# Performance work log

Measured on AMD Instinct MI355X. Metric: run time of the kernel, lower is better.

## Reference

```python
import jax, jax.numpy as jnp
import numpy as np

B, H, L, D = 2, 16, 2048, 64


def setup_inputs() -> dict:
    key = jax.random.key(0)
    kq, kk, kv, km = jax.random.split(key, 4)
    q = jax.random.normal(kq, (B, H, L, D), dtype=jnp.float32)
    k = jax.random.normal(kk, (B, H, L, D), dtype=jnp.float32)
    v = jax.random.normal(kv, (B, H, L, D), dtype=jnp.float32)
    mask = jax.random.uniform(km, (B, L, L), dtype=jnp.float32)
    return {"q": q, "k": k, "v": v, "mask": mask}


def reference(q, k, v, mask):
    d_tensor = k.shape[-1]
    # score = q @ k^T / sqrt(d)  -> [B,H,L,L]
    score = jnp.einsum("bhqd,bhkd->bhqk", q, k) / jnp.sqrt(jnp.float32(d_tensor))
    # multiplicative mask, broadcast over heads (mask: [B,L,L] -> [B,1,L,L])
    score = score * mask[:, None, :, :]
    score = jax.nn.softmax(score, axis=-1)
    out = jnp.einsum("bhqk,bhkd->bhqd", score, v)
    return (out, score)
```

## Files before the change

### kernel.cpp

```cpp
#include <hip/hip_runtime.h>

typedef __attribute__((ext_vector_type(8))) short bf16x8;
typedef __attribute__((ext_vector_type(4))) float f32x4;
typedef __attribute__((ext_vector_type(4))) unsigned u32x4;

#define DEV static __device__ __forceinline__

constexpr int B_ = 2, H_ = 16, L_ = 2048, D_ = 64;
constexpr float SCALE = 0.125f;

DEV short f2bf(float f) {
  unsigned u = __builtin_bit_cast(unsigned, f);
  u += 0x7fffu + ((u >> 16) & 1u);
  return (short)(u >> 16);
}
DEV unsigned pk2(float lo, float hi) {
  return (unsigned)(unsigned short)f2bf(lo) | ((unsigned)(unsigned short)f2bf(hi) << 16);
}
DEV float bflo(unsigned u) { return __builtin_bit_cast(float, u << 16); }
DEV float bfhi(unsigned u) { return __builtin_bit_cast(float, u & 0xffff0000u); }

DEV bf16x8 frag_from(const float* src) {
  float4 f0 = *(const float4*)src;
  float4 f1 = *(const float4*)(src + 4);
  bf16x8 r;
  r[0] = f2bf(f0.x); r[1] = f2bf(f0.y); r[2] = f2bf(f0.z); r[3] = f2bf(f0.w);
  r[4] = f2bf(f1.x); r[5] = f2bf(f1.y); r[6] = f2bf(f1.z); r[7] = f2bf(f1.w);
  return r;
}

__global__ __launch_bounds__(256) void convert_k_kernel(
    const float* __restrict__ Kg, short* __restrict__ Kp) {
  const int tid = threadIdx.x;
  const int lane = tid & 63, half = (tid >> 6) & 1, sub = tid >> 7;
  const int blk = blockIdx.x;
  const int bh = blk >> 6;
  const int ktile = (((blk & 63) << 1) | sub);
  const int g = lane >> 4, ln = lane & 15;
  const float* src = Kg + ((size_t)bh * L_ + ktile * 16 + ln) * D_ + half * 32 + g * 8;
  bf16x8 f = frag_from(src);
  *(bf16x8*)(Kp + ((((size_t)(bh * 128 + ktile)) * 2 + half) * 64 + lane) * 8) = f;
}

__global__ __launch_bounds__(256) void convert_vp_kernel(
    const float* __restrict__ Vg, short* __restrict__ Vp) {
  __shared__ short vt[64 * 256];
  const int tid = threadIdx.x;
  const int bh = blockIdx.x >> 3, c = blockIdx.x & 7;
  const float* vb = Vg + (size_t)bh * L_ * D_ + (size_t)c * 256 * D_;
  const int ka = (tid & 127) * 2, dh = (tid >> 7) * 32;
  const float* r0 = vb + (size_t)ka * D_ + dh;
  const float* r1 = r0 + D_;
#pragma unroll
  for (int i = 0; i < 8; ++i) {
    float4 a = *(const float4*)(r0 + i * 4);
    float4 b = *(const float4*)(r1 + i * 4);
    unsigned p0 = pk2(a.x, b.x), p1 = pk2(a.y, b.y), p2 = pk2(a.z, b.z), p3 = pk2(a.w, b.w);
    const int dd = dh + i * 4;
    *(unsigned*)((char*)vt + (dd + 0) * 512 + ((ka * 2) ^ (((dd + 0) & 7) << 4))) = p0;
    *(unsigned*)((char*)vt + (dd + 1) * 512 + ((ka * 2) ^ (((dd + 1) & 7) << 4))) = p1;
    *(unsigned*)((char*)vt + (dd + 2) * 512 + ((ka * 2) ^ (((dd + 2) & 7) << 4))) = p2;
    *(unsigned*)((char*)vt + (dd + 3) * 512 + ((ka * 2) ^ (((dd + 3) & 7) << 4))) = p3;
  }
  __syncthreads();
  u32x4* out = (u32x4*)Vp + (size_t)(bh * 8 + c) * 2048;
#pragma unroll
  for (int i = 0; i < 8; ++i) {
    const int u = tid + 256 * i;
    const int lane = u & 63, w = (u >> 6) & 7, n = u >> 9;
    const int g = lane >> 4, ln = lane & 15;
    const int d = n * 16 + ln;
    const int kb = (w * 16 + g * 4) * 2;
    const char* rowp = (const char*)vt + d * 512;
    const int swz = (d & 7) << 4;
    uint2 lo = *(const uint2*)(rowp + (kb ^ swz));
    uint2 hi = *(const uint2*)(rowp + ((kb + 256) ^ swz));
    out[u] = u32x4{lo.x, lo.y, hi.x, hi.y};
  }
}

template <bool USEPRE>
__global__ __launch_bounds__(512, 2) void attn_fused(
    const float* __restrict__ Qg, const float* __restrict__ Kg,
    const short* __restrict__ Kp, const float* __restrict__ Vg,
    const short* __restrict__ Vpg, const float* __restrict__ Mg,
    float* __restrict__ Pg, float* __restrict__ Og) {
  const int tid = threadIdx.x;
  const int w = tid >> 6, lane = tid & 63;
  const int g = lane >> 4, ln = lane & 15;

  const int bid = blockIdx.x;
  const int wg = (bid & 7) * 512 + (bid >> 3);
  const int q0 = (wg & 127) << 4;
  const int bh = wg >> 7;
  const int b = bh >> 4;

  __shared__ float red_o[128 * 64];
  __shared__ float red[8][16];

  const float* qp = Qg + (size_t)bh * L_ * D_;
  const float* mrow = Mg + (size_t)b * L_ * L_ + (size_t)(q0 + ln) * L_;
  float* prow = Pg + (size_t)bh * L_ * L_ + (size_t)(q0 + ln) * L_;

  bf16x8 qf0 = frag_from(qp + (size_t)(q0 + ln) * D_ + g * 8);
  bf16x8 qf1 = frag_from(qp + (size_t)(q0 + ln) * D_ + 32 + g * 8);

  unsigned pkv[32];
  float mx = -1e30f;
  const bf16x8* kpb = (const bf16x8*)Kp + ((size_t)bh * 128 + w) * 128 + lane;

#pragma unroll
  for (int j = 0; j < 16; ++j) {
    bf16x8 k0, k1;
    if (USEPRE) {
      k0 = kpb[j * 1024];
      k1 = kpb[j * 1024 + 64];
    } else {
      const float* kr = Kg + (size_t)bh * L_ * D_ + (size_t)((w + 8 * j) * 16 + ln) * D_;
      k0 = frag_from(kr + g * 8);
      k1 = frag_from(kr + 32 + g * 8);
    }
    f32x4 acc{0.f, 0.f, 0.f, 0.f};
    acc = __builtin_amdgcn_mfma_f32_16x16x32_bf16(k0, qf0, acc, 0, 0, 0);
    acc = __builtin_amdgcn_mfma_f32_16x16x32_bf16(k1, qf1, acc, 0, 0, 0);
    float4 mk = *(const float4*)(mrow + (w + 8 * j) * 16 + g * 4);
    float l0 = acc[0] * SCALE * mk.x;
    float l1 = acc[1] * SCALE * mk.y;
    float l2 = acc[2] * SCALE * mk.z;
    float l3 = acc[3] * SCALE * mk.w;
    mx = fmaxf(mx, fmaxf(fmaxf(l0, l1), fmaxf(l2, l3)));
    pkv[2 * j] = pk2(l0, l1);
    pkv[2 * j + 1] = pk2(l2, l3);
  }

  mx = fmaxf(mx, __shfl_xor(mx, 16));
  mx = fmaxf(mx, __shfl_xor(mx, 32));
  if (lane < 16) red[w][ln] = mx;
  __syncthreads();
  {
    float t = red[0][ln];
#pragma unroll
    for (int ww = 1; ww < 8; ++ww) t = fmaxf(t, red[ww][ln]);
    mx = t;
  }
  float sm = 0.f;
#pragma unroll
  for (int j = 0; j < 16; ++j) {
    float e0 = __expf(bflo(pkv[2 * j]) - mx);
    float e1 = __expf(bfhi(pkv[2 * j]) - mx);
    float e2 = __expf(bflo(pkv[2 * j + 1]) - mx);
    float e3 = __expf(bfhi(pkv[2 * j + 1]) - mx);
    sm += (e0 + e1) + (e2 + e3);
    pkv[2 * j] = pk2(e0, e1);
    pkv[2 * j + 1] = pk2(e2, e3);
  }
  sm += __shfl_xor(sm, 16);
  sm += __shfl_xor(sm, 32);
  __syncthreads();
  if (lane < 16) red[w][ln] = sm;
  __syncthreads();
  float inv;
  {
    float t = red[0][ln];
#pragma unroll
    for (int ww = 1; ww < 8; ++ww) t += red[ww][ln];
    inv = 1.0f / t;
  }

#pragma unroll
  for (int j = 0; j < 16; ++j) {
    float n0 = bflo(pkv[2 * j]) * inv, n1 = bfhi(pkv[2 * j]) * inv;
    float n2 = bflo(pkv[2 * j + 1]) * inv, n3 = bfhi(pkv[2 * j + 1]) * inv;
    f32x4 st{n0, n1, n2, n3};
    __builtin_nontemporal_store(st, (f32x4*)(prow + (w + 8 * j) * 16 + g * 4));
    pkv[2 * j] = pk2(n0, n1);
    pkv[2 * j + 1] = pk2(n2, n3);
  }

  f32x4 acc_o[4];
#pragma unroll
  for (int n = 0; n < 4; ++n) acc_o[n] = f32x4{0.f, 0.f, 0.f, 0.f};

  const u32x4* vp4 = (const u32x4*)Vpg + (size_t)bh * 8 * 2048;

#pragma unroll
  for (int c = 0; c < 8; ++c) {
    u32x4 au{pkv[4 * c], pkv[4 * c + 1], pkv[4 * c + 2], pkv[4 * c + 3]};
    bf16x8 pa = __builtin_bit_cast(bf16x8, au);
#pragma unroll
    for (int n = 0; n < 4; ++n) {
      bf16x8 bf;
      if (USEPRE) {
        bf = __builtin_bit_cast(bf16x8, vp4[(size_t)c * 2048 + (n * 8 + w) * 64 + lane]);
      } else {
        const int d = n * 16 + ln;
        const int k0 = c * 256 + w * 16 + g * 4;
        const float* vb = Vg + (size_t)bh * L_ * D_ + d;
#pragma unroll
        for (int e = 0; e < 4; ++e) bf[e] = f2bf(vb[(size_t)(k0 + e) * D_]);
#pragma unroll
        for (int e = 0; e < 4; ++e) bf[4 + e] = f2bf(vb[(size_t)(k0 + 128 + e) * D_]);
      }
      acc_o[n] = __builtin_amdgcn_mfma_f32_16x16x32_bf16(pa, bf, acc_o[n], 0, 0, 0);
    }
  }

#pragma unroll
  for (int n = 0; n < 4; ++n)
#pragma unroll
    for (int r = 0; r < 4; ++r)
      red_o[(w * 16 + g * 4 + r) * 64 + n * 16 + ln] = acc_o[n][r];
  __syncthreads();
  {
    float* ob = Og + (size_t)bh * L_ * D_ + (size_t)q0 * D_;
    const int row = tid >> 5, dp = (tid & 31) * 2;
    float s0 = 0.f, s1 = 0.f;
#pragma unroll
    for (int ww = 0; ww < 8; ++ww) {
      s0 += red_o[(ww * 16 + row) * 64 + dp];
      s1 += red_o[(ww * 16 + row) * 64 + dp + 1];
    }
    __builtin_nontemporal_store(s0, ob + row * D_ + dp);
    __builtin_nontemporal_store(s1, ob + row * D_ + dp + 1);
  }
}

extern "C" void kernel_launch(void* const* d_in, const int* in_sizes, int n_in,
                              void* d_out, int out_size, void* d_ws, size_t ws_size,
                              hipStream_t stream) {
  const float* q = (const float*)d_in[0];
  const float* k = (const float*)d_in[1];
  const float* v = (const float*)d_in[2];
  const float* mask = (const float*)d_in[3];
  float* out = (float*)d_out;
  float* score = out + (size_t)B_ * H_ * L_ * D_;

  const size_t elems = (size_t)B_ * H_ * L_ * D_;
  const size_t need = elems * 2 * sizeof(short);
  const int nblk = B_ * H_ * (L_ / 16);

  if (ws_size >= need) {
    short* kp = (short*)d_ws;
    short* vp = kp + elems;
    convert_k_kernel<<<2048, 256, 0, stream>>>(k, kp);
    convert_vp_kernel<<<B_ * H_ * 8, 256, 0, stream>>>(v, vp);
    attn_fused<true><<<nblk, 512, 0, stream>>>(q, k, kp, v, vp, mask, score, out);
  } else {
    attn_fused<false><<<nblk, 512, 0, stream>>>(q, k, nullptr, v, nullptr, mask, score, out);
  }
}
```

Before: 288.5 us.

## Remap key tiles per wave, prefetch V fragments, fuse normalization into PV loop

```diff
diff --git a/kernel.cpp b/kernel.cpp
--- a/kernel.cpp
+++ b/kernel.cpp
@@ -39,7 +39,7 @@
   const int g = lane >> 4, ln = lane & 15;
   const float* src = Kg + ((size_t)bh * L_ + ktile * 16 + ln) * D_ + half * 32 + g * 8;
   bf16x8 f = frag_from(src);
-  *(bf16x8*)(Kp + ((((size_t)(bh * 128 + ktile)) * 2 + half) * 64 + lane) * 8) = f;
+  *(bf16x8*)(Kp + ((size_t)bh * 16384 + ktile * 128 + half * 64 + lane) * 8) = f;
 }
 
 __global__ __launch_bounds__(256) void convert_vp_kernel(
@@ -70,11 +70,11 @@
     const int lane = u & 63, w = (u >> 6) & 7, n = u >> 9;
     const int g = lane >> 4, ln = lane & 15;
     const int d = n * 16 + ln;
-    const int kb = (w * 16 + g * 4) * 2;
+    const int kb = (w * 32 + g * 4) * 2;
     const char* rowp = (const char*)vt + d * 512;
     const int swz = (d & 7) << 4;
     uint2 lo = *(const uint2*)(rowp + (kb ^ swz));
-    uint2 hi = *(const uint2*)(rowp + ((kb + 256) ^ swz));
+    uint2 hi = *(const uint2*)(rowp + ((kb + 32) ^ swz));
     out[u] = u32x4{lo.x, lo.y, hi.x, hi.y};
   }
 }
@@ -107,23 +107,24 @@
 
   unsigned pkv[32];
   float mx = -1e30f;
-  const bf16x8* kpb = (const bf16x8*)Kp + ((size_t)bh * 128 + w) * 128 + lane;
+  const bf16x8* kb_ = (const bf16x8*)Kp + (size_t)bh * 16384 + lane;
 
 #pragma unroll
   for (int j = 0; j < 16; ++j) {
+    const int tile = 2 * w + ((j >> 1) << 4) + (j & 1);
     bf16x8 k0, k1;
     if (USEPRE) {
-      k0 = kpb[j * 1024];
-      k1 = kpb[j * 1024 + 64];
+      k0 = kb_[tile * 128];
+      k1 = kb_[tile * 128 + 64];
     } else {
-      const float* kr = Kg + (size_t)bh * L_ * D_ + (size_t)((w + 8 * j) * 16 + ln) * D_;
+      const float* kr = Kg + (size_t)bh * L_ * D_ + (size_t)(tile * 16 + ln) * D_;
       k0 = frag_from(kr + g * 8);
       k1 = frag_from(kr + 32 + g * 8);
     }
     f32x4 acc{0.f, 0.f, 0.f, 0.f};
     acc = __builtin_amdgcn_mfma_f32_16x16x32_bf16(k0, qf0, acc, 0, 0, 0);
     acc = __builtin_amdgcn_mfma_f32_16x16x32_bf16(k1, qf1, acc, 0, 0, 0);
-    float4 mk = *(const float4*)(mrow + (w + 8 * j) * 16 + g * 4);
+    float4 mk = *(const float4*)(mrow + tile * 16 + g * 4);
     float l0 = acc[0] * SCALE * mk.x;
     float l1 = acc[1] * SCALE * mk.y;
     float l2 = acc[2] * SCALE * mk.z;
@@ -131,6 +132,15 @@
     mx = fmaxf(mx, fmaxf(fmaxf(l0, l1), fmaxf(l2, l3)));
     pkv[2 * j] = pk2(l0, l1);
     pkv[2 * j + 1] = pk2(l2, l3);
+  }
+
+  const u32x4* vp4 = (const u32x4*)Vpg + (size_t)bh * 8 * 2048;
+  bf16x8 vb0, vb1, vb2, vb3;
+  if (USEPRE) {
+    vb0 = __builtin_bit_cast(bf16x8, vp4[(0 * 8 + w) * 64 + lane]);
+    vb1 = __builtin_bit_cast(bf16x8, vp4[(1 * 8 + w) * 64 + lane]);
+    vb2 = __builtin_bit_cast(bf16x8, vp4[(2 * 8 + w) * 64 + lane]);
+    vb3 = __builtin_bit_cast(bf16x8, vp4[(3 * 8 + w) * 64 + lane]);
   }
 
   mx = fmaxf(mx, __shfl_xor(mx, 16));
@@ -167,42 +177,52 @@
     inv = 1.0f / t;
   }
 
-#pragma unroll
-  for (int j = 0; j < 16; ++j) {
-    float n0 = bflo(pkv[2 * j]) * inv, n1 = bfhi(pkv[2 * j]) * inv;
-    float n2 = bflo(pkv[2 * j + 1]) * inv, n3 = bfhi(pkv[2 * j + 1]) * inv;
-    f32x4 st{n0, n1, n2, n3};
-    __builtin_nontemporal_store(st, (f32x4*)(prow + (w + 8 * j) * 16 + g * 4));
-    pkv[2 * j] = pk2(n0, n1);
-    pkv[2 * j + 1] = pk2(n2, n3);
-  }
-
   f32x4 acc_o[4];
 #pragma unroll
   for (int n = 0; n < 4; ++n) acc_o[n] = f32x4{0.f, 0.f, 0.f, 0.f};
 
-  const u32x4* vp4 = (const u32x4*)Vpg + (size_t)bh * 8 * 2048;
+  const float* vsrc_f32 = Vg + (size_t)bh * L_ * D_;
 
 #pragma unroll
   for (int c = 0; c < 8; ++c) {
-    u32x4 au{pkv[4 * c], pkv[4 * c + 1], pkv[4 * c + 2], pkv[4 * c + 3]};
+    unsigned u0 = pkv[4 * c], u1 = pkv[4 * c + 1], u2 = pkv[4 * c + 2], u3 = pkv[4 * c + 3];
+    float n0 = bflo(u0) * inv, n1 = bfhi(u0) * inv;
+    float n2 = bflo(u1) * inv, n3 = bfhi(u1) * inv;
+    float n4 = bflo(u2) * inv, n5 = bfhi(u2) * inv;
+    float n6 = bflo(u3) * inv, n7 = bfhi(u3) * inv;
+    const int te = 2 * w + 16 * c;
+    f32x4 s0{n0, n1, n2, n3};
+    f32x4 s1{n4, n5, n6, n7};
+    __builtin_nontemporal_store(s0, (f32x4*)(prow + te * 16 + g * 4));
+    __builtin_nontemporal_store(s1, (f32x4*)(prow + (te + 1) * 16 + g * 4));
+    u32x4 au{pk2(n0, n1), pk2(n2, n3), pk2(n4, n5), pk2(n6, n7)};
     bf16x8 pa = __builtin_bit_cast(bf16x8, au);
-#pragma unroll
-    for (int n = 0; n < 4; ++n) {
-      bf16x8 bf;
-      if (USEPRE) {
-        bf = __builtin_bit_cast(bf16x8, vp4[(size_t)c * 2048 + (n * 8 + w) * 64 + lane]);
-      } else {
+    bf16x8 c0 = vb0, c1 = vb1, c2 = vb2, c3 = vb3;
+    if (USEPRE) {
+      if (c < 7) {
+        vb0 = __builtin_bit_cast(bf16x8, vp4[(size_t)(c + 1) * 2048 + (0 * 8 + w) * 64 + lane]);
+        vb1 = __builtin_bit_cast(bf16x8, vp4[(size_t)(c + 1) * 2048 + (1 * 8 + w) * 64 + lane]);
+        vb2 = __builtin_bit_cast(bf16x8, vp4[(size_t)(c + 1) * 2048 + (2 * 8 + w) * 64 + lane]);
+        vb3 = __builtin_bit_cast(bf16x8, vp4[(size_t)(c + 1) * 2048 + (3 * 8 + w) * 64 + lane]);
+      }
+    } else {
+      const int k0i = c * 256 + w * 32 + g * 4;
+#pragma unroll
+      for (int n = 0; n < 4; ++n) {
         const int d = n * 16 + ln;
-        const int k0 = c * 256 + w * 16 + g * 4;
-        const float* vb = Vg + (size_t)bh * L_ * D_ + d;
-#pragma unroll
-        for (int e = 0; e < 4; ++e) bf[e] = f2bf(vb[(size_t)(k0 + e) * D_]);
-#pragma unroll
-        for (int e = 0; e < 4; ++e) bf[4 + e] = f2bf(vb[(size_t)(k0 + 128 + e) * D_]);
+        const float* vbp = vsrc_f32 + d;
+        bf16x8 bf;
+#pragma unroll
+        for (int e = 0; e < 4; ++e) bf[e] = f2bf(vbp[(size_t)(k0i + e) * D_]);
+#pragma unroll
+        for (int e = 0; e < 4; ++e) bf[4 + e] = f2bf(vbp[(size_t)(k0i + 16 + e) * D_]);
+        if (n == 0) c0 = bf; else if (n == 1) c1 = bf; else if (n == 2) c2 = bf; else c3 = bf;
       }
-      acc_o[n] = __builtin_amdgcn_mfma_f32_16x16x32_bf16(pa, bf, acc_o[n], 0, 0, 0);
     }
+    acc_o[0] = __builtin_amdgcn_mfma_f32_16x16x32_bf16(pa, c0, acc_o[0], 0, 0, 0);
+    acc_o[1] = __builtin_amdgcn_mfma_f32_16x16x32_bf16(pa, c1, acc_o[1], 0, 0, 0);
+    acc_o[2] = __builtin_amdgcn_mfma_f32_16x16x32_bf16(pa, c2, acc_o[2], 0, 0, 0);
+    acc_o[3] = __builtin_amdgcn_mfma_f32_16x16x32_bf16(pa, c3, acc_o[3], 0, 0, 0);
   }
 
 #pragma unroll
```

Result: no change. 290.4 us (+0.6%).
